# Kernel tuning notes

Measured on AMD Instinct MI355X. Metric: run time of the kernel, lower is better.

The kernel has to match this reference:

```python
import jax, jax.numpy as jnp
import numpy as np


def setup_inputs() -> dict:
    key = jax.random.key(0)
    k = jax.random.split(key, 5)
    B, L, D = 8, 2048, 256  # D = 2*d_model, c_len == q_len == L (required by source's s1 broadcast)
    c = jax.random.normal(k[0], (B, L, D), dtype=jnp.float32)
    q = jax.random.normal(k[1], (B, L, D), dtype=jnp.float32)
    c_weight = jax.random.normal(k[2], (D, 1), dtype=jnp.float32) * 0.05
    q_weight = jax.random.normal(k[3], (D, 1), dtype=jnp.float32) * 0.05
    cq_weight = jax.random.normal(k[4], (1, 1, D), dtype=jnp.float32) * 0.05
    bias = jnp.zeros((1,), dtype=jnp.float32)
    return {"c": c, "q": q, "c_weight": c_weight, "q_weight": q_weight,
            "cq_weight": cq_weight, "bias": bias}


def reference(c, q, c_weight, q_weight, cq_weight, bias):
    # Dropout omitted (identity) for a deterministic reference.
    # s0: [B, c_len, 1] -> broadcasts over q_len
    s0 = jnp.matmul(c, c_weight)                       # [B, L, 1]
    # s1 (faithful to source, which uses c here): [B, 1, c_len]
    s1 = jnp.swapaxes(jnp.matmul(c, q_weight), 1, 2)   # [B, 1, L]
    # s2: elementwise-scaled batched GEMM: [B, c_len, q_len]
    s2 = jnp.matmul(c * cq_weight, jnp.swapaxes(q, 1, 2))
    s = s0 + s1 + s2 + bias                            # broadcast sum + scalar bias
    return s
```

## Files before the change

### kernel.cpp

```cpp
#include <hip/hip_runtime.h>
#include <hip/hip_bf16.h>

#define B_ 8
#define L_ 2048
#define D_ 256

typedef __bf16 bf16x8 __attribute__((ext_vector_type(8)));
typedef float f32x4 __attribute__((ext_vector_type(4)));

static __device__ __forceinline__ unsigned short f2bf(float f) {
    unsigned int u = __builtin_bit_cast(unsigned int, f);
    unsigned int lsb = (u >> 16) & 1u;
    u += 0x7fffu + lsb;
    return (unsigned short)(u >> 16);
}

static __device__ __forceinline__ void gload_lds16(const void* g, void* l) {
    __builtin_amdgcn_global_load_lds(
        (const __attribute__((address_space(1))) unsigned int*)g,
        (__attribute__((address_space(3))) unsigned int*)l, 16, 0, 0);
}

__global__ __launch_bounds__(256) void prep_kernel(
    const float* __restrict__ c, const float* __restrict__ q,
    const float* __restrict__ cw, const float* __restrict__ qw,
    const float* __restrict__ cqw, const float* __restrict__ bias,
    unsigned short* __restrict__ Abf, unsigned short* __restrict__ Qbf,
    float* __restrict__ s0, float* __restrict__ s1)
{
    const int wave = threadIdx.x >> 6;
    const int lane = threadIdx.x & 63;
    const int row  = blockIdx.x * 4 + wave;

    const float4 cv  = *(const float4*)(c   + (size_t)row * D_ + lane * 4);
    const float4 qv  = *(const float4*)(q   + (size_t)row * D_ + lane * 4);
    const float4 wc  = *(const float4*)(cw  + lane * 4);
    const float4 wq  = *(const float4*)(qw  + lane * 4);
    const float4 wcq = *(const float4*)(cqw + lane * 4);

    ushort4 av, qb;
    av.x = f2bf(cv.x * wcq.x); av.y = f2bf(cv.y * wcq.y);
    av.z = f2bf(cv.z * wcq.z); av.w = f2bf(cv.w * wcq.w);
    qb.x = f2bf(qv.x); qb.y = f2bf(qv.y);
    qb.z = f2bf(qv.z); qb.w = f2bf(qv.w);
    *(ushort4*)(Abf + (size_t)row * D_ + lane * 4) = av;
    *(ushort4*)(Qbf + (size_t)row * D_ + lane * 4) = qb;

    float p0 = cv.x * wc.x + cv.y * wc.y + cv.z * wc.z + cv.w * wc.w;
    float p1 = cv.x * wq.x + cv.y * wq.y + cv.z * wq.z + cv.w * wq.w;
    #pragma unroll
    for (int off = 32; off > 0; off >>= 1) {
        p0 += __shfl_down(p0, off);
        p1 += __shfl_down(p1, off);
    }
    if (lane == 0) { s0[row] = p0 + bias[0]; s1[row] = p1; }
}

#define BM 128
#define BN 128
#define BK 32
#define NSTEP (D_ / BK)

__global__ __launch_bounds__(256) void gemm_kernel(
    const unsigned short* __restrict__ A, const unsigned short* __restrict__ Q,
    const float* __restrict__ s0, const float* __restrict__ s1,
    float* __restrict__ out)
{
    __shared__ __align__(16) unsigned short As[3][BM * BK];
    __shared__ __align__(16) unsigned short Qs[3][BM * BK];

    const int tid  = threadIdx.x;
    const int wave = tid >> 6;
    const int lane = tid & 63;

    const int lin = blockIdx.x + (blockIdx.y << 4) + (blockIdx.z << 8);
    const int nl  = ((lin & 7) << 8) | (lin >> 3);
    const int b   = nl >> 8;
    const int brow = ((nl >> 4) & 15) * BM;
    const int bcol = (nl & 15) * BN;

    const unsigned short* Ab = A + ((size_t)b * L_ + brow) * D_;
    const unsigned short* Qb = Q + ((size_t)b * L_ + bcol) * D_;

    const int wr = wave >> 1;
    const int wc = wave & 1;

    float s0v[4];
    #pragma unroll
    for (int m = 0; m < 4; ++m)
        s0v[m] = s0[(size_t)b * L_ + brow + wr * 64 + m * 16 + (lane & 15)];
    f32x4 s1v[4];
    #pragma unroll
    for (int n = 0; n < 4; ++n)
        #pragma unroll
        for (int r = 0; r < 4; ++r)
            s1v[n][r] = s1[(size_t)b * L_ + bcol + wc * 64 + n * 16 + (lane >> 4) * 4 + r];

    f32x4 acc[4][4];
    #pragma unroll
    for (int m = 0; m < 4; ++m)
        #pragma unroll
        for (int n = 0; n < 4; ++n)
            #pragma unroll
            for (int r = 0; r < 4; ++r)
                acc[m][n][r] = s0v[m] + s1v[n][r];

    auto stage = [&](int s) {
        const int k0 = s * BK;
        unsigned short* ab = &As[s % 3][0];
        unsigned short* qb = &Qs[s % 3][0];
        #pragma unroll
        for (int i = 0; i < 2; ++i) {
            const int sidx = i * 256 + wave * 64 + lane;
            const int row  = sidx >> 2;
            const int sl   = sidx & 3;
            const int ksrc = k0 + ((sl ^ ((row >> 1) & 3)) << 3);
            const int wbase = (i * 256 + wave * 64) * 8;
            gload_lds16(Ab + (size_t)row * D_ + ksrc, ab + wbase);
            gload_lds16(Qb + (size_t)row * D_ + ksrc, qb + wbase);
        }
    };

    auto compute = [&](int t) {
        const unsigned short* ab = &As[t % 3][0];
        const unsigned short* qb = &Qs[t % 3][0];
        bf16x8 af[4], qf[4];
        #pragma unroll
        for (int m = 0; m < 4; ++m) {
            const int row = wr * 64 + m * 16 + (lane & 15);
            const int idx = row * 32 + (((lane >> 4) ^ ((row >> 1) & 3)) << 3);
            af[m] = *(const bf16x8*)(ab + idx);
        }
        #pragma unroll
        for (int n = 0; n < 4; ++n) {
            const int row = wc * 64 + n * 16 + (lane & 15);
            const int idx = row * 32 + (((lane >> 4) ^ ((row >> 1) & 3)) << 3);
            qf[n] = *(const bf16x8*)(qb + idx);
        }
        __builtin_amdgcn_s_setprio(1);
        #pragma unroll
        for (int m = 0; m < 4; ++m)
            #pragma unroll
            for (int n = 0; n < 4; ++n)
                acc[m][n] = __builtin_amdgcn_mfma_f32_16x16x32_bf16(
                    qf[n], af[m], acc[m][n], 0, 0, 0);
        __builtin_amdgcn_s_setprio(0);
    };

    stage(0);
    stage(1);

#define STEP(T, VM) do {                                        \
        if ((T) + 2 < NSTEP) stage((T) + 2);                    \
        asm volatile("s_waitcnt vmcnt(" #VM ")" ::: "memory");  \
        __builtin_amdgcn_s_barrier();                           \
        asm volatile("" ::: "memory");                          \
        compute(T);                                             \
        asm volatile("" ::: "memory");                          \
        __builtin_amdgcn_s_barrier();                           \
        asm volatile("" ::: "memory");                          \
    } while (0)

    STEP(0, 8); STEP(1, 8); STEP(2, 8); STEP(3, 8);
    STEP(4, 8); STEP(5, 8); STEP(6, 4); STEP(7, 0);
#undef STEP

    float* outb = out + ((size_t)b * L_ + brow) * L_ + bcol;
    #pragma unroll
    for (int m = 0; m < 4; ++m) {
        const int row = wr * 64 + m * 16 + (lane & 15);
        float* rp = outb + (size_t)row * L_ + wc * 64 + (lane >> 4) * 4;
        #pragma unroll
        for (int n = 0; n < 4; ++n)
            *(f32x4*)(rp + n * 16) = acc[m][n];
    }
}

__global__ void naive_kernel(const float* __restrict__ c, const float* __restrict__ q,
                             const float* __restrict__ cw, const float* __restrict__ qw,
                             const float* __restrict__ cqw, const float* __restrict__ bias,
                             float* __restrict__ out)
{
    const size_t total = (size_t)B_ * L_ * L_;
    for (size_t idx = (size_t)blockIdx.x * blockDim.x + threadIdx.x; idx < total;
         idx += (size_t)gridDim.x * blockDim.x) {
        const int b = (int)(idx / ((size_t)L_ * L_));
        const int rem = (int)(idx % ((size_t)L_ * L_));
        const int i = rem / L_, j = rem % L_;
        const float* ci = c + ((size_t)b * L_ + i) * D_;
        const float* cj = c + ((size_t)b * L_ + j) * D_;
        const float* qj = q + ((size_t)b * L_ + j) * D_;
        float acc = bias[0];
        for (int d = 0; d < D_; ++d)
            acc += ci[d] * cw[d] + cj[d] * qw[d] + ci[d] * cqw[d] * qj[d];
        out[idx] = acc;
    }
}

extern "C" void kernel_launch(void* const* d_in, const int* in_sizes, int n_in,
                              void* d_out, int out_size, void* d_ws, size_t ws_size,
                              hipStream_t stream) {
    const float* c    = (const float*)d_in[0];
    const float* q    = (const float*)d_in[1];
    const float* cw   = (const float*)d_in[2];
    const float* qw   = (const float*)d_in[3];
    const float* cqw  = (const float*)d_in[4];
    const float* bias = (const float*)d_in[5];
    float* out = (float*)d_out;

    const size_t bytesA = (size_t)B_ * L_ * D_ * 2;
    const size_t need   = 2 * bytesA + 2 * (size_t)B_ * L_ * 4;

    if (ws_size >= need) {
        unsigned short* Abf = (unsigned short*)d_ws;
        unsigned short* Qbf = (unsigned short*)((char*)d_ws + bytesA);
        float* s0 = (float*)((char*)d_ws + 2 * bytesA);
        float* s1 = s0 + (size_t)B_ * L_;
        prep_kernel<<<B_ * L_ / 4, 256, 0, stream>>>(c, q, cw, qw, cqw, bias,
                                                     Abf, Qbf, s0, s1);
        dim3 grid(L_ / BN, L_ / BM, B_);
        gemm_kernel<<<grid, 256, 0, stream>>>(Abf, Qbf, s0, s1, out);
    } else {
        naive_kernel<<<2048, 256, 0, stream>>>(c, q, cw, qw, cqw, bias, out);
    }
}
```

Before: 53.42 us.

## Load Q fragments directly into registers, bypassing LDS, and swap MFMA operand roles

The Q tile is no longer staged through shared memory. Each wave loads its Q fragments straight from global memory into double-buffered registers one step ahead, which halves LDS traffic and footprint and adds an occupancy hint of 3 blocks per CU. The MFMA operands are swapped, so the accumulator layout transposes: the bias vectors are re-indexed and the output is written as scalar 4-byte stores, coalesced across 16 lanes, instead of 16-byte vector stores. The risks are more redundant global loads of Q (each wave pair loads it separately), exposed global latency on the register loads, and a less efficient store pattern for the large output.

```diff
diff --git a/kernel.cpp b/kernel.cpp
--- a/kernel.cpp
+++ b/kernel.cpp
@@ -61,13 +61,12 @@
 #define BK 32
 #define NSTEP (D_ / BK)
 
-__global__ __launch_bounds__(256) void gemm_kernel(
+__global__ __launch_bounds__(256, 3) void gemm_kernel(
     const unsigned short* __restrict__ A, const unsigned short* __restrict__ Q,
     const float* __restrict__ s0, const float* __restrict__ s1,
     float* __restrict__ out)
 {
     __shared__ __align__(16) unsigned short As[3][BM * BK];
-    __shared__ __align__(16) unsigned short Qs[3][BM * BK];
 
     const int tid  = threadIdx.x;
     const int wave = tid >> 6;
@@ -85,16 +84,21 @@
     const int wr = wave >> 1;
     const int wc = wave & 1;
 
-    float s0v[4];
+    const unsigned short* qp[4];
+    #pragma unroll
+    for (int n = 0; n < 4; ++n)
+        qp[n] = Qb + (size_t)(wc * 64 + n * 16 + (lane & 15)) * D_ + (lane >> 4) * 8;
+
+    float s0v[4][4];
     #pragma unroll
     for (int m = 0; m < 4; ++m)
-        s0v[m] = s0[(size_t)b * L_ + brow + wr * 64 + m * 16 + (lane & 15)];
-    f32x4 s1v[4];
+        #pragma unroll
+        for (int r = 0; r < 4; ++r)
+            s0v[m][r] = s0[(size_t)b * L_ + brow + wr * 64 + m * 16 + (lane >> 4) * 4 + r];
+    float s1v[4];
     #pragma unroll
     for (int n = 0; n < 4; ++n)
-        #pragma unroll
-        for (int r = 0; r < 4; ++r)
-            s1v[n][r] = s1[(size_t)b * L_ + bcol + wc * 64 + n * 16 + (lane >> 4) * 4 + r];
+        s1v[n] = s1[(size_t)b * L_ + bcol + wc * 64 + n * 16 + (lane & 15)];
 
     f32x4 acc[4][4];
     #pragma unroll
@@ -103,12 +107,13 @@
         for (int n = 0; n < 4; ++n)
             #pragma unroll
             for (int r = 0; r < 4; ++r)
-                acc[m][n][r] = s0v[m] + s1v[n][r];
-
-    auto stage = [&](int s) {
+                acc[m][n][r] = s0v[m][r] + s1v[n];
+
+    bf16x8 qreg[2][4];
+
+    auto stageA = [&](int s) {
         const int k0 = s * BK;
         unsigned short* ab = &As[s % 3][0];
-        unsigned short* qb = &Qs[s % 3][0];
         #pragma unroll
         for (int i = 0; i < 2; ++i) {
             const int sidx = i * 256 + wave * 64 + lane;
@@ -117,62 +122,66 @@
             const int ksrc = k0 + ((sl ^ ((row >> 1) & 3)) << 3);
             const int wbase = (i * 256 + wave * 64) * 8;
             gload_lds16(Ab + (size_t)row * D_ + ksrc, ab + wbase);
-            gload_lds16(Qb + (size_t)row * D_ + ksrc, qb + wbase);
         }
     };
 
-    auto compute = [&](int t) {
-        const unsigned short* ab = &As[t % 3][0];
-        const unsigned short* qb = &Qs[t % 3][0];
-        bf16x8 af[4], qf[4];
-        #pragma unroll
-        for (int m = 0; m < 4; ++m) {
-            const int row = wr * 64 + m * 16 + (lane & 15);
-            const int idx = row * 32 + (((lane >> 4) ^ ((row >> 1) & 3)) << 3);
-            af[m] = *(const bf16x8*)(ab + idx);
-        }
-        #pragma unroll
-        for (int n = 0; n < 4; ++n) {
-            const int row = wc * 64 + n * 16 + (lane & 15);
-            const int idx = row * 32 + (((lane >> 4) ^ ((row >> 1) & 3)) << 3);
-            qf[n] = *(const bf16x8*)(qb + idx);
-        }
-        __builtin_amdgcn_s_setprio(1);
-        #pragma unroll
-        for (int m = 0; m < 4; ++m)
-            #pragma unroll
-            for (int n = 0; n < 4; ++n)
-                acc[m][n] = __builtin_amdgcn_mfma_f32_16x16x32_bf16(
-                    qf[n], af[m], acc[m][n], 0, 0, 0);
-        __builtin_amdgcn_s_setprio(0);
-    };
-
-    stage(0);
-    stage(1);
+#define QLOAD(T) do {                                                        \
+        _Pragma("unroll")                                                    \
+        for (int n_ = 0; n_ < 4; ++n_)                                       \
+            qreg[(T) & 1][n_] = *(const bf16x8*)(qp[n_] + (T) * BK);         \
+    } while (0)
+
+#define COMPUTE(T) do {                                                      \
+        const unsigned short* ab_ = &As[(T) % 3][0];                         \
+        bf16x8 af_[4];                                                       \
+        _Pragma("unroll")                                                    \
+        for (int m_ = 0; m_ < 4; ++m_) {                                     \
+            const int row_ = wr * 64 + m_ * 16 + (lane & 15);                \
+            const int idx_ = row_ * 32 + (((lane >> 4) ^ ((row_ >> 1) & 3)) << 3); \
+            af_[m_] = *(const bf16x8*)(ab_ + idx_);                          \
+        }                                                                    \
+        __builtin_amdgcn_s_setprio(1);                                       \
+        _Pragma("unroll")                                                    \
+        for (int m_ = 0; m_ < 4; ++m_)                                       \
+            _Pragma("unroll")                                                \
+            for (int n_ = 0; n_ < 4; ++n_)                                   \
+                acc[m_][n_] = __builtin_amdgcn_mfma_f32_16x16x32_bf16(       \
+                    af_[m_], qreg[(T) & 1][n_], acc[m_][n_], 0, 0, 0);       \
+        __builtin_amdgcn_s_setprio(0);                                       \
+    } while (0)
+
+    stageA(0);
+    QLOAD(0);
+    stageA(1);
 
 #define STEP(T, VM) do {                                        \
-        if ((T) + 2 < NSTEP) stage((T) + 2);                    \
+        if ((T) + 2 < NSTEP) stageA((T) + 2);                   \
+        if ((T) + 1 < NSTEP) QLOAD((T) + 1);                    \
         asm volatile("s_waitcnt vmcnt(" #VM ")" ::: "memory");  \
         __builtin_amdgcn_s_barrier();                           \
-        asm volatile("" ::: "memory");                          \
-        compute(T);                                             \
+        COMPUTE(T);                                             \
         asm volatile("" ::: "memory");                          \
         __builtin_amdgcn_s_barrier();                           \
         asm volatile("" ::: "memory");                          \
     } while (0)
 
     STEP(0, 8); STEP(1, 8); STEP(2, 8); STEP(3, 8);
-    STEP(4, 8); STEP(5, 8); STEP(6, 4); STEP(7, 0);
+    STEP(4, 8); STEP(5, 8); STEP(6, 6); STEP(7, 0);
 #undef STEP
+#undef COMPUTE
+#undef QLOAD
 
     float* outb = out + ((size_t)b * L_ + brow) * L_ + bcol;
     #pragma unroll
     for (int m = 0; m < 4; ++m) {
-        const int row = wr * 64 + m * 16 + (lane & 15);
-        float* rp = outb + (size_t)row * L_ + wc * 64 + (lane >> 4) * 4;
-        #pragma unroll
-        for (int n = 0; n < 4; ++n)
-            *(f32x4*)(rp + n * 16) = acc[m][n];
+        #pragma unroll
+        for (int r = 0; r < 4; ++r) {
+            const int row = wr * 64 + m * 16 + (lane >> 4) * 4 + r;
+            float* rp = outb + (size_t)row * L_;
+            #pragma unroll
+            for (int n = 0; n < 4; ++n)
+                rp[wc * 64 + n * 16 + (lane & 15)] = acc[m][n][r];
+        }
     }
 }
 
```

After: 57.90 us. 8.4% more time.
